# Optimization experiments

Measured on AMD Instinct MI355X. Metric: run time of the kernel, lower is better.

The kernel has to match this reference:

```python
import jax, jax.numpy as jnp
import numpy as np

D_MODEL = 1024
N_HEADS = 16
D_K = D_MODEL // N_HEADS
THETA = 10000.0
NEG_INF = -1e30


def _rope_tables(token_positions, d_k, theta=THETA):
    # freqs[t, i] = t / theta**(2i/d_k), i in [0, d_k/2)
    exponent = jnp.arange(0, d_k, 2, dtype=jnp.float32)  # [d_k/2]
    inv_freq = 1.0 / theta ** (exponent / d_k)
    freqs = token_positions.astype(jnp.float32)[:, None] * inv_freq[None, :]  # [s, d_k/2]
    return jnp.cos(freqs), jnp.sin(freqs)


def _apply_rope(x, cos, sin):
    # x: [..., s, d_k]; interleaved pair rotation (pairs are (x[2i], x[2i+1]))
    x1 = x[..., 0::2]
    x2 = x[..., 1::2]
    r1 = x1 * cos - x2 * sin
    r2 = x1 * sin + x2 * cos
    return jnp.stack([r1, r2], axis=-1).reshape(x.shape)


def setup_inputs() -> dict:
    key = jax.random.key(0)
    ks = jax.random.split(key, 5)
    b, s = 2, 2048
    scale = np.sqrt(2.0 / (D_MODEL + D_MODEL))
    return {
        "x": jax.random.normal(ks[0], (b, s, D_MODEL), dtype=jnp.float32),
        "Wq": jax.random.normal(ks[1], (D_MODEL, D_MODEL), dtype=jnp.float32) * scale,
        "Wk": jax.random.normal(ks[2], (D_MODEL, D_MODEL), dtype=jnp.float32) * scale,
        "Wv": jax.random.normal(ks[3], (D_MODEL, D_MODEL), dtype=jnp.float32) * scale,
        "Wo": jax.random.normal(ks[4], (D_MODEL, D_MODEL), dtype=jnp.float32) * scale,
        "token_positions": jnp.arange(s, dtype=jnp.int64 if jax.config.jax_enable_x64 else jnp.int32),
    }


def reference(x, Wq, Wk, Wv, Wo, token_positions):
    b, s, _ = x.shape
    # QKV projections: weight stored [in, out]
    q = jnp.einsum('bsi,io->bso', x, Wq)
    k = jnp.einsum('bsi,io->bso', x, Wk)
    v = jnp.einsum('bsi,io->bso', x, Wv)
    # split heads: [b, h, s, d_k]
    q = q.reshape(b, s, N_HEADS, D_K).transpose(0, 2, 1, 3)
    k = k.reshape(b, s, N_HEADS, D_K).transpose(0, 2, 1, 3)
    v = v.reshape(b, s, N_HEADS, D_K).transpose(0, 2, 1, 3)
    # RoPE
    cos, sin = _rope_tables(token_positions, D_K)
    q = _apply_rope(q, cos, sin)
    k = _apply_rope(k, cos, sin)
    # causal attention with full materialized scores (faithful to source)
    scores = jnp.einsum('bhid,bhjd->bhij', q, k) / jnp.sqrt(jnp.float32(D_K))
    mask = jnp.tril(jnp.ones((s, s), dtype=bool))
    scores = jnp.where(mask, scores, NEG_INF)
    probs = jax.nn.softmax(scores, axis=-1)
    out = jnp.einsum('bhij,bhjd->bhid', probs, v)
    out = out.transpose(0, 2, 1, 3).reshape(b, s, D_MODEL)
    return jnp.einsum('bsi,io->bso', out, Wo)
```

## Files before the change

kernel.cpp:

```cpp
#include <hip/hip_runtime.h>
#include <hip/hip_bf16.h>
#include <cmath>

#define S_LEN 2048
#define DMODEL 1024
#define NHEADS 16
#define DK 64
#define BATCH 2
#define MTOT (BATCH * S_LEN)

using short8 = __attribute__((ext_vector_type(8))) short;
using floatx4 = __attribute__((ext_vector_type(4))) float;

__device__ __forceinline__ unsigned short f2b(float f) {
    union { float f; unsigned u; } v; v.f = f;
    unsigned r = v.u + 0x7fff + ((v.u >> 16) & 1);
    return (unsigned short)(r >> 16);
}

__device__ __forceinline__ unsigned pack2(float a, float b) {
    float2 t; t.x = a; t.y = b;
    __hip_bfloat162 h = __float22bfloat162_rn(t);
    union { __hip_bfloat162 h; unsigned u; } v; v.h = h;
    return v.u;
}

__device__ __forceinline__ void gload16(const void* g, void* l) {
    __builtin_amdgcn_global_load_lds(
        (const __attribute__((address_space(1))) unsigned int*)g,
        (__attribute__((address_space(3))) unsigned int*)l, 16, 0, 0);
}

#define FENCE() asm volatile("" ::: "memory")

__global__ __launch_bounds__(256) void prep_k(
    const float* __restrict__ x, unsigned short* __restrict__ xb,
    const int* __restrict__ tokpos, float* __restrict__ ct, float* __restrict__ st,
    const float* W0, const float* W1, const float* W2, const float* W3,
    unsigned short* T0, unsigned short* T1, unsigned short* T2, unsigned short* T3) {
    __shared__ float t[64][65];
    const int b = blockIdx.x;
    if (b < 2048) {
        int i = (b * 256 + threadIdx.x) * 8;
        float4 a = *(const float4*)(x + i);
        float4 bb = *(const float4*)(x + i + 4);
        short8 o;
        o[0] = f2b(a.x); o[1] = f2b(a.y); o[2] = f2b(a.z); o[3] = f2b(a.w);
        o[4] = f2b(bb.x); o[5] = f2b(bb.y); o[6] = f2b(bb.z); o[7] = f2b(bb.w);
        *(short8*)(xb + i) = o;
    } else if (b < 2304) {
        int idx = (b - 2048) * 256 + threadIdx.x;
        int si = idx >> 5;
        int ip = idx & 31;
        float pos = (float)tokpos[si];
        float inv_freq = powf(10000.0f, -(float)(2 * ip) / 64.0f);
        float ang = pos * inv_freq;
        ct[idx] = cosf(ang);
        st[idx] = sinf(ang);
    } else {
        int id = b - 2304;
        int z = id >> 8;
        int bx = id & 15, by = (id >> 4) & 15;
        const float* W = z == 0 ? W0 : z == 1 ? W1 : z == 2 ? W2 : W3;
        unsigned short* T = z == 0 ? T0 : z == 1 ? T1 : z == 2 ? T2 : T3;
        const bool perm = (z < 2);
        int n0 = bx * 64, k0 = by * 64;
        int rr = threadIdx.x >> 6, cc = threadIdx.x & 63;
#pragma unroll
        for (int r = 0; r < 16; r++) {
            int row = r * 4 + rr;
            t[row][cc] = W[(size_t)(k0 + row) * DMODEL + n0 + cc];
        }
        __syncthreads();
#pragma unroll
        for (int r = 0; r < 16; r++) {
            int row = r * 4 + rr;
            int drow = perm ? (((row & 1) ? 32 : 0) + (row >> 1)) : row;
            T[(size_t)(n0 + drow) * DMODEL + k0 + cc] = f2b(t[cc][row]);
        }
    }
}

__global__ __launch_bounds__(256) void add_k(float* __restrict__ out,
                                             const float* __restrict__ p) {
    int i = (blockIdx.x * 256 + threadIdx.x) * 8;
    float4 a = *(const float4*)(out + i);
    float4 b = *(const float4*)(p + i);
    float4 c = *(const float4*)(out + i + 4);
    float4 d = *(const float4*)(p + i + 4);
    a.x += b.x; a.y += b.y; a.z += b.z; a.w += b.w;
    c.x += d.x; c.y += d.y; c.z += d.z; c.w += d.w;
    *(float4*)(out + i) = a;
    *(float4*)(out + i + 4) = c;
}

__global__ __launch_bounds__(256) void vtrans_k(const unsigned short* __restrict__ V,
                                                unsigned short* __restrict__ Vt) {
    __shared__ unsigned short t[64][72];
    const int tid = threadIdx.x;
    const int s0 = blockIdx.x * 64, d0 = blockIdx.y * 64;
    const int bb = s0 >> 11;
#pragma unroll
    for (int it = 0; it < 4; it++) {
        int e = (it * 256 + tid) * 4;
        int r = e >> 6, c = e & 63;
        *(ushort4*)&t[r][c] = *(const ushort4*)(V + (size_t)(s0 + r) * DMODEL + d0 + c);
    }
    __syncthreads();
#pragma unroll
    for (int it = 0; it < 4; it++) {
        int e = (it * 256 + tid) * 4;
        int r = e >> 6, c = e & 63;
        ushort4 v;
        v.x = t[c + 0][r]; v.y = t[c + 1][r];
        v.z = t[c + 2][r]; v.w = t[c + 3][r];
        *(ushort4*)(Vt + (size_t)(bb * 1024 + d0 + r) * S_LEN + (s0 & (S_LEN - 1)) + c) = v;
    }
}

__global__ __launch_bounds__(512, 2) void mm_k(
    const unsigned short* __restrict__ A,
    const unsigned short* __restrict__ Bt0, const unsigned short* __restrict__ Bt1,
    const unsigned short* __restrict__ Bt2,
    void* C0, void* C1, void* C2,
    const float* __restrict__ ct, const float* __restrict__ st, int kind) {
    __shared__ __align__(16) unsigned short blob[10 * 8192];

    const int z = blockIdx.z;
    const unsigned short* Bt = (kind == 1) ? Bt0 : (z == 0 ? Bt0 : z == 1 ? Bt1 : Bt2);
    void* C = (kind == 1) ? (z == 0 ? C0 : C1) : (z == 0 ? C0 : z == 1 ? C1 : C2);
    const int mode = (kind == 1) ? 0 : (z == 2 ? 3 : 1);
    const int t0 = (kind == 1) ? z * 8 : 0;
    const int NT = (kind == 1) ? 8 : 16;
    const float qscale = (z == 0 && kind == 0) ? 0.18033688011112042f : 1.0f;

    const int tid = threadIdx.x;
    const int w = tid >> 6, lane = tid & 63;
    const int l15 = lane & 15, quad = lane >> 4;
    const int wr = w >> 2, wc = w & 3;
    const int m0 = blockIdx.x * 256, n0 = blockIdx.y * 256;

    const int rbase = (w >> 1) * 16 + l15;
    const int cbase = (w & 1) * 32 + quad * 8;

    floatx4 acc[8][4];
#pragma unroll
    for (int i = 0; i < 8; i++)
#pragma unroll
        for (int j = 0; j < 4; j++) acc[i][j] = (floatx4){0.f, 0.f, 0.f, 0.f};

    auto stage_half = [&](int h) {
        const int ts = t0 + (h >> 2), part = h & 3;
        const int slot = h % 10;
        const unsigned short* src =
            (part < 2 ? A + (((size_t)(m0 + part * 128 + rbase)) << 10)
                      : Bt + (((size_t)(n0 + (part - 2) * 128 + rbase)) << 10))
            + (size_t)ts * 64 + cbase;
        char* d = (char*)blob + slot * 16384 + w * 1024;
        gload16(src, d);
        gload16(src + (64 << 10), d + 8192);
    };

#pragma unroll
    for (int h = 0; h < 6; ++h) stage_half(h);
    asm volatile("s_waitcnt vmcnt(4)" ::: "memory");
    FENCE(); __builtin_amdgcn_s_barrier(); FENCE();

    short8 af[4][2];
    for (int t = 0; t < NT; ++t) {
        const int sb = (4 * t) % 10;
        int sA = sb + wr;            if (sA >= 10) sA -= 10;
        int sB = sb + 2 + (wc >> 1); if (sB >= 10) sB -= 10;
        const char* LA = (const char*)blob + sA * 16384;
        const char* LB = (const char*)blob + sB * 16384;
#pragma unroll
        for (int q = 0; q < 4; ++q) {
            const int rh = q >> 1, ch = q & 1;
            if (ch == 0) {
#pragma unroll
                for (int ii = 0; ii < 4; ++ii)
#pragma unroll
                    for (int kh = 0; kh < 2; ++kh)
                        af[ii][kh] = *(const short8*)(LA + ((rh * 4 + ii) * 2 + kh) * 1024 + lane * 16);
            }
            short8 bf[2][2];
#pragma unroll
            for (int jj = 0; jj < 2; ++jj)
#pragma unroll
                for (int kh = 0; kh < 2; ++kh)
                    bf[jj][kh] = *(const short8*)(LB + (((wc & 1) * 4 + ch * 2 + jj) * 2 + kh) * 1024 + lane * 16);
            const int h = 4 * t + q + 6;
            if (h < 4 * NT) stage_half(h);
            if (q == 3) {
                if (t == NT - 2) asm volatile("s_waitcnt vmcnt(0)" ::: "memory");
                else             asm volatile("s_waitcnt vmcnt(4)" ::: "memory");
            }
            FENCE(); __builtin_amdgcn_s_barrier(); FENCE();
            __builtin_amdgcn_s_setprio(1);
#pragma unroll
            for (int ii = 0; ii < 4; ++ii)
#pragma unroll
                for (int jj = 0; jj < 2; ++jj) {
                    floatx4 a0 = acc[rh * 4 + ii][ch * 2 + jj];
                    a0 = __builtin_amdgcn_mfma_f32_16x16x32_bf16(af[ii][0], bf[jj][0], a0, 0, 0, 0);
                    a0 = __builtin_amdgcn_mfma_f32_16x16x32_bf16(af[ii][1], bf[jj][1], a0, 0, 0, 0);
                    acc[rh * 4 + ii][ch * 2 + jj] = a0;
                }
            __builtin_amdgcn_s_setprio(0);
            FENCE(); __builtin_amdgcn_s_barrier(); FENCE();
        }
    }

#pragma unroll
    for (int i = 0; i < 8; i++) {
        const int rowb = m0 + wr * 128 + i * 16 + quad * 4;
        if (mode == 0) {
            float* Cf = (float*)C;
#pragma unroll
            for (int j = 0; j < 4; j++) {
                int colb = n0 + wc * 64 + j * 16 + l15;
#pragma unroll
                for (int r = 0; r < 4; r++)
                    Cf[(size_t)(rowb + r) * DMODEL + colb] = acc[i][j][r];
            }
        } else if (mode == 1) {
            unsigned short* Cb = (unsigned short*)C;
#pragma unroll
            for (int jh = 0; jh < 2; jh++) {
                int ip = jh * 16 + l15;
                int cole = n0 + wc * 64 + jh * 16 + l15;
#pragma unroll
                for (int r = 0; r < 4; r++) {
                    int row = rowb + r;
                    int si = row & (S_LEN - 1);
                    float c = ct[si * 32 + ip] * qscale;
                    float s = st[si * 32 + ip] * qscale;
                    float e = acc[i][jh][r];
                    float od = acc[i][jh + 2][r];
                    Cb[(size_t)row * DMODEL + cole] = f2b(e * c - od * s);
                    Cb[(size_t)row * DMODEL + cole + 32] = f2b(e * s + od * c);
                }
            }
        } else {
            unsigned short* Cb = (unsigned short*)C;
#pragma unroll
            for (int j = 0; j < 4; j++) {
                int colb = n0 + wc * 64 + j * 16 + l15;
#pragma unroll
                for (int r = 0; r < 4; r++)
                    Cb[(size_t)(rowb + r) * DMODEL + colb] = f2b(acc[i][j][r]);
            }
        }
    }
}

__global__ __launch_bounds__(256) void attn_k(const unsigned short* __restrict__ Q,
                                              const unsigned short* __restrict__ K,
                                              const unsigned short* __restrict__ Vt,
                                              unsigned short* __restrict__ O) {
    __shared__ __align__(16) unsigned short Kblob[2][4096];
    __shared__ __align__(16) unsigned short Vblob[2][4096];
    __shared__ __align__(16) unsigned short Ps[4][32 * 72];

    const int tid = threadIdx.x;
    const int w = tid >> 6, lane = tid & 63;
    const int l15 = lane & 15, quad = lane >> 4;
    const int idx = blockIdx.x;
    const int qt = 15 - (idx >> 5);
    const int bh = idx & 31;
    const int bb = bh >> 4, h = bh & 15;
    const int qb_w = qt * 128 + w * 32;

    short8 aq[2][2];
#pragma unroll
    for (int qg = 0; qg < 2; qg++) {
        const size_t qoff = (size_t)(bb * S_LEN + qb_w + qg * 16 + l15) * DMODEL + h * DK;
        aq[qg][0] = *(const short8*)(Q + qoff + quad * 8);
        aq[qg][1] = *(const short8*)(Q + qoff + 32 + quad * 8);
    }

    floatx4 o[2][4];
#pragma unroll
    for (int qg = 0; qg < 2; qg++)
#pragma unroll
        for (int f = 0; f < 4; f++) o[qg][f] = (floatx4){0.f, 0.f, 0.f, 0.f};
    float mv[2] = {-1e30f, -1e30f}, lv[2] = {0.f, 0.f};

    const unsigned short* Kb = K + (size_t)(bb * S_LEN) * DMODEL + h * DK;
    const unsigned short* Vb = Vt + (size_t)(bb * 1024 + h * DK) * S_LEN;
    unsigned short* ps = &Ps[w][0];

    auto stage = [&](int b, int kb) {
#pragma unroll
        for (int it = 0; it < 4; it++) {
            int g = it * 4 + w;
            if (g < 8) {
                const unsigned short* gp =
                    Kb + (size_t)(kb + (g >> 1) * 16 + l15) * DMODEL + (g & 1) * 32 + quad * 8;
                gload16(gp, (char*)&Kblob[b][0] + g * 1024);
            } else {
                int gv = g - 8;
                const unsigned short* gp =
                    Vb + (size_t)((gv >> 1) * 16 + l15) * S_LEN + kb + (gv & 1) * 32 + quad * 8;
                gload16(gp, (char*)&Vblob[b][0] + gv * 1024);
            }
        }
    };

    const int nkt = 2 * qt + 2;
    stage(0, 0);
    for (int kt = 0; kt < nkt; kt++) {
        const int b = kt & 1;
        const int kb = kt * 64;
        __syncthreads();
        if (kt + 1 < nkt) stage(b ^ 1, (kt + 1) * 64);

        if (kb <= qb_w + 31) {
            const unsigned short* kbb = &Kblob[b][0];
            floatx4 c[4][2];
            __builtin_amdgcn_s_setprio(1);
#pragma unroll
            for (int g = 0; g < 4; g++) {
                short8 kf0 = *(const short8*)(kbb + (g * 2 + 0) * 512 + lane * 8);
                short8 kf1 = *(const short8*)(kbb + (g * 2 + 1) * 512 + lane * 8);
#pragma unroll
                for (int qg = 0; qg < 2; qg++) {
                    floatx4 t = {0.f, 0.f, 0.f, 0.f};
                    t = __builtin_amdgcn_mfma_f32_16x16x32_bf16(kf0, aq[qg][0], t, 0, 0, 0);
                    c[g][qg] = __builtin_amdgcn_mfma_f32_16x16x32_bf16(kf1, aq[qg][1], t, 0, 0, 0);
                }
            }
            __builtin_amdgcn_s_setprio(0);

#pragma unroll
            for (int qg = 0; qg < 2; qg++) {
                const int qbg = qb_w + qg * 16;
                const int qrow = qbg + l15;
                float sv[16];
                if (kb + 63 <= qbg) {
#pragma unroll
                    for (int g = 0; g < 4; g++)
#pragma unroll
                        for (int r = 0; r < 4; r++) sv[g * 4 + r] = c[g][qg][r];
                } else {
#pragma unroll
                    for (int g = 0; g < 4; g++)
#pragma unroll
                        for (int r = 0; r < 4; r++) {
                            int key = kb + g * 16 + quad * 4 + r;
                            sv[g * 4 + r] = (key <= qrow) ? c[g][qg][r] : -1e30f;
                        }
                }
                float t0 = fmaxf(fmaxf(sv[0], sv[1]), sv[2]);
                float t1 = fmaxf(fmaxf(sv[3], sv[4]), sv[5]);
                float t2 = fmaxf(fmaxf(sv[6], sv[7]), sv[8]);
                float t3 = fmaxf(fmaxf(sv[9], sv[10]), sv[11]);
                float t4 = fmaxf(fmaxf(sv[12], sv[13]), sv[14]);
                float mx = fmaxf(fmaxf(fmaxf(t0, t1), fmaxf(t2, t3)), fmaxf(t4, sv[15]));
                mx = fmaxf(mx, __shfl_xor(mx, 16));
                mx = fmaxf(mx, __shfl_xor(mx, 32));

                if (!__all(mx <= mv[qg])) {
                    float mnew = fmaxf(mv[qg], mx);
                    float alpha = exp2f(mv[qg] - mnew);
                    mv[qg] = mnew;
                    lv[qg] *= alpha;
#pragma unroll
                    for (int f = 0; f < 4; f++) {
                        o[qg][f][0] *= alpha; o[qg][f][1] *= alpha;
                        o[qg][f][2] *= alpha; o[qg][f][3] *= alpha;
                    }
                }
                float p[16], psum = 0.f;
#pragma unroll
                for (int i = 0; i < 16; i++) {
                    p[i] = exp2f(sv[i] - mv[qg]);
                    psum += p[i];
                }
                lv[qg] += psum;

#pragma unroll
                for (int g = 0; g < 4; g++) {
                    uint2 pk;
                    pk.x = pack2(p[g * 4 + 0], p[g * 4 + 1]);
                    pk.y = pack2(p[g * 4 + 2], p[g * 4 + 3]);
                    *(uint2*)(ps + (qg * 16 + l15) * 72 + g * 16 + quad * 4) = pk;
                }
            }

            short8 pf[2][2];
#pragma unroll
            for (int qg = 0; qg < 2; qg++) {
                pf[qg][0] = *(const short8*)(ps + (qg * 16 + l15) * 72 + quad * 8);
                pf[qg][1] = *(const short8*)(ps + (qg * 16 + l15) * 72 + 32 + quad * 8);
            }
            const unsigned short* vbb = &Vblob[b][0];
            __builtin_amdgcn_s_setprio(1);
#pragma unroll
            for (int f = 0; f < 4; f++) {
                short8 vf0 = *(const short8*)(vbb + (f * 2 + 0) * 512 + lane * 8);
                short8 vf1 = *(const short8*)(vbb + (f * 2 + 1) * 512 + lane * 8);
#pragma unroll
                for (int qg = 0; qg < 2; qg++) {
                    o[qg][f] = __builtin_amdgcn_mfma_f32_16x16x32_bf16(vf0, pf[qg][0], o[qg][f], 0, 0, 0);
                    o[qg][f] = __builtin_amdgcn_mfma_f32_16x16x32_bf16(vf1, pf[qg][1], o[qg][f], 0, 0, 0);
                }
            }
            __builtin_amdgcn_s_setprio(0);
        }
    }

#pragma unroll
    for (int qg = 0; qg < 2; qg++) {
        lv[qg] += __shfl_xor(lv[qg], 16);
        lv[qg] += __shfl_xor(lv[qg], 32);
        float inv = 1.0f / lv[qg];
#pragma unroll
        for (int f = 0; f < 4; f++) {
            uint2 pk;
            pk.x = pack2(o[qg][f][0] * inv, o[qg][f][1] * inv);
            pk.y = pack2(o[qg][f][2] * inv, o[qg][f][3] * inv);
            *(uint2*)(ps + (qg * 16 + l15) * 72 + f * 16 + quad * 4) = pk;
        }
        short8 r0 = *(const short8*)(ps + (qg * 16 + l15) * 72 + quad * 8);
        short8 r1 = *(const short8*)(ps + (qg * 16 + l15) * 72 + 32 + quad * 8);
        size_t obase = (size_t)(bb * S_LEN + qb_w + qg * 16 + l15) * DMODEL + h * DK;
        *(short8*)(O + obase + quad * 8) = r0;
        *(short8*)(O + obase + 32 + quad * 8) = r1;
    }
}

extern "C" void kernel_launch(void* const* d_in, const int* in_sizes, int n_in,
                              void* d_out, int out_size, void* d_ws,
                              size_t ws_size, hipStream_t stream) {
    const float* x = (const float*)d_in[0];
    const float* Wq = (const float*)d_in[1];
    const float* Wk = (const float*)d_in[2];
    const float* Wv = (const float*)d_in[3];
    const float* Wo = (const float*)d_in[4];
    const int* tokpos = (const int*)d_in[5];
    float* out = (float*)d_out;

    const size_t MD = (size_t)MTOT * DMODEL;
    const size_t WD = (size_t)DMODEL * DMODEL;
    unsigned short* xb = (unsigned short*)d_ws;
    unsigned short* Wqt = xb + MD;
    unsigned short* Wkt = Wqt + WD;
    unsigned short* Wvt = Wkt + WD;
    unsigned short* Wot = Wvt + WD;
    unsigned short* Q = Wot + WD;
    unsigned short* K = Q + MD;
    unsigned short* V = K + MD;
    unsigned short* Vt = V + MD;
    float* ct = (float*)(Vt + MD);
    float* st = ct + S_LEN * 32;
    unsigned short* O = V;
    float* P1 = (float*)Q;

    prep_k<<<dim3(3328), dim3(256), 0, stream>>>(x, xb, tokpos, ct, st,
                                                 Wq, Wk, Wv, Wo, Wqt, Wkt, Wvt, Wot);

    mm_k<<<dim3(16, 4, 3), dim3(512), 0, stream>>>(xb, Wqt, Wkt, Wvt,
                                                   (void*)Q, (void*)K, (void*)V, ct, st, 0);
    vtrans_k<<<dim3(64, 16), dim3(256), 0, stream>>>(V, Vt);
    attn_k<<<dim3(512), dim3(256), 0, stream>>>(Q, K, Vt, O);
    mm_k<<<dim3(16, 4, 2), dim3(512), 0, stream>>>(O, Wot, Wot, Wot,
                                                   (void*)out, (void*)P1, (void*)P1, ct, st, 1);
    add_k<<<dim3(2048), dim3(256), 0, stream>>>(out, P1);
}
```

Measured before the change: 230.2 us.

## Rebalance causal attention with 256-row tiles, split-KV for long rows, and merge kernel

Attention blocks now cover 256 query rows with 8 waves, and a static table assigns each block a key range. The longest query tiles are split into two key-range halves whose unnormalized partial outputs and max/sum stats go to workspace, and a new merge kernel combines them. The aim is to even out causal work across 352 blocks (11 per batch-head) so the tail of long blocks does not dominate. The cost is an extra kernel launch, fp32 partial-result traffic, and workspace reuse of the xb buffer.

```diff
diff --git a/kernel.cpp b/kernel.cpp
--- a/kernel.cpp
+++ b/kernel.cpp
@@ -254,22 +254,30 @@
     }
 }
 
-__global__ __launch_bounds__(256) void attn_k(const unsigned short* __restrict__ Q,
+__global__ __launch_bounds__(512) void attn_k(const unsigned short* __restrict__ Q,
                                               const unsigned short* __restrict__ K,
                                               const unsigned short* __restrict__ Vt,
-                                              unsigned short* __restrict__ O) {
+                                              unsigned short* __restrict__ O,
+                                              float* __restrict__ Ub,
+                                              float* __restrict__ MLb) {
     __shared__ __align__(16) unsigned short Kblob[2][4096];
     __shared__ __align__(16) unsigned short Vblob[2][4096];
-    __shared__ __align__(16) unsigned short Ps[4][32 * 72];
+    __shared__ __align__(16) unsigned short Ps[8][16 * 72];
+
+    static const int T_j[11]  = {4, 7, 7, 3, 6, 6, 5, 5, 2, 1, 0};
+    static const int T_k0[11] = {0, 0, 16, 0, 0, 14, 0, 12, 0, 0, 0};
+    static const int T_k1[11] = {20, 16, 32, 16, 14, 28, 12, 24, 12, 8, 4};
+    static const int T_sx[11] = {-1, 0, 1, -1, 2, 3, 4, 5, -1, -1, -1};
 
     const int tid = threadIdx.x;
     const int w = tid >> 6, lane = tid & 63;
     const int l15 = lane & 15, quad = lane >> 4;
     const int idx = blockIdx.x;
-    const int qt = 15 - (idx >> 5);
+    const int sr = idx >> 5;
     const int bh = idx & 31;
     const int bb = bh >> 4, h = bh & 15;
-    const int qb_w = qt * 128 + w * 32;
+    const int j = T_j[sr], kt0 = T_k0[sr], kt1 = T_k1[sr], sx = T_sx[sr];
+    const int qb_w = j * 256 + w * 32;
 
     short8 aq[2][2];
 #pragma unroll
@@ -292,8 +300,8 @@
 
     auto stage = [&](int b, int kb) {
 #pragma unroll
-        for (int it = 0; it < 4; it++) {
-            int g = it * 4 + w;
+        for (int it = 0; it < 2; it++) {
+            int g = it * 8 + w;
             if (g < 8) {
                 const unsigned short* gp =
                     Kb + (size_t)(kb + (g >> 1) * 16 + l15) * DMODEL + (g & 1) * 32 + quad * 8;
@@ -307,13 +315,12 @@
         }
     };
 
-    const int nkt = 2 * qt + 2;
-    stage(0, 0);
-    for (int kt = 0; kt < nkt; kt++) {
-        const int b = kt & 1;
+    stage(0, kt0 * 64);
+    for (int kt = kt0; kt < kt1; kt++) {
+        const int b = (kt - kt0) & 1;
         const int kb = kt * 64;
         __syncthreads();
-        if (kt + 1 < nkt) stage(b ^ 1, (kt + 1) * 64);
+        if (kt + 1 < kt1) stage(b ^ 1, (kt + 1) * 64);
 
         if (kb <= qb_w + 31) {
             const unsigned short* kbb = &Kblob[b][0];
@@ -332,6 +339,7 @@
             }
             __builtin_amdgcn_s_setprio(0);
 
+            short8 pf[2][2];
 #pragma unroll
             for (int qg = 0; qg < 2; qg++) {
                 const int qbg = qb_w + qg * 16;
@@ -384,16 +392,12 @@
                     uint2 pk;
                     pk.x = pack2(p[g * 4 + 0], p[g * 4 + 1]);
                     pk.y = pack2(p[g * 4 + 2], p[g * 4 + 3]);
-                    *(uint2*)(ps + (qg * 16 + l15) * 72 + g * 16 + quad * 4) = pk;
-                }
-            }
-
-            short8 pf[2][2];
-#pragma unroll
-            for (int qg = 0; qg < 2; qg++) {
-                pf[qg][0] = *(const short8*)(ps + (qg * 16 + l15) * 72 + quad * 8);
-                pf[qg][1] = *(const short8*)(ps + (qg * 16 + l15) * 72 + 32 + quad * 8);
-            }
+                    *(uint2*)(ps + l15 * 72 + g * 16 + quad * 4) = pk;
+                }
+                pf[qg][0] = *(const short8*)(ps + l15 * 72 + quad * 8);
+                pf[qg][1] = *(const short8*)(ps + l15 * 72 + 32 + quad * 8);
+            }
+
             const unsigned short* vbb = &Vblob[b][0];
             __builtin_amdgcn_s_setprio(1);
 #pragma unroll
@@ -410,24 +414,89 @@
         }
     }
 
-#pragma unroll
-    for (int qg = 0; qg < 2; qg++) {
-        lv[qg] += __shfl_xor(lv[qg], 16);
-        lv[qg] += __shfl_xor(lv[qg], 32);
-        float inv = 1.0f / lv[qg];
-#pragma unroll
-        for (int f = 0; f < 4; f++) {
-            uint2 pk;
-            pk.x = pack2(o[qg][f][0] * inv, o[qg][f][1] * inv);
-            pk.y = pack2(o[qg][f][2] * inv, o[qg][f][3] * inv);
-            *(uint2*)(ps + (qg * 16 + l15) * 72 + f * 16 + quad * 4) = pk;
-        }
-        short8 r0 = *(const short8*)(ps + (qg * 16 + l15) * 72 + quad * 8);
-        short8 r1 = *(const short8*)(ps + (qg * 16 + l15) * 72 + 32 + quad * 8);
-        size_t obase = (size_t)(bb * S_LEN + qb_w + qg * 16 + l15) * DMODEL + h * DK;
-        *(short8*)(O + obase + quad * 8) = r0;
-        *(short8*)(O + obase + 32 + quad * 8) = r1;
-    }
+    if (sx >= 0) {
+        const int slot = sx * 32 + bh;
+#pragma unroll
+        for (int qg = 0; qg < 2; qg++) {
+            float* up = Ub + (size_t)slot * 16384 + (tid * 2 + qg) * 16;
+#pragma unroll
+            for (int f = 0; f < 4; f++) {
+                float4 v; v.x = o[qg][f][0]; v.y = o[qg][f][1];
+                v.z = o[qg][f][2]; v.w = o[qg][f][3];
+                *(float4*)(up + f * 4) = v;
+            }
+            float* mlp = MLb + (size_t)slot * 2048 + (tid * 2 + qg) * 2;
+            mlp[0] = mv[qg];
+            mlp[1] = lv[qg];
+        }
+    } else {
+        __syncthreads();
+#pragma unroll
+        for (int qg = 0; qg < 2; qg++) {
+            float l = lv[qg];
+            l += __shfl_xor(l, 16);
+            l += __shfl_xor(l, 32);
+            float inv = 1.0f / l;
+#pragma unroll
+            for (int f = 0; f < 4; f++) {
+                uint2 pk;
+                pk.x = pack2(o[qg][f][0] * inv, o[qg][f][1] * inv);
+                pk.y = pack2(o[qg][f][2] * inv, o[qg][f][3] * inv);
+                *(uint2*)(ps + l15 * 72 + f * 16 + quad * 4) = pk;
+            }
+            short8 r0 = *(const short8*)(ps + l15 * 72 + quad * 8);
+            short8 r1 = *(const short8*)(ps + l15 * 72 + 32 + quad * 8);
+            size_t obase = (size_t)(bb * S_LEN + qb_w + qg * 16 + l15) * DMODEL + h * DK;
+            *(short8*)(O + obase + quad * 8) = r0;
+            *(short8*)(O + obase + 32 + quad * 8) = r1;
+        }
+    }
+}
+
+__global__ __launch_bounds__(512) void mrg_k(const float* __restrict__ Ub,
+                                             const float* __restrict__ MLb,
+                                             unsigned short* __restrict__ O) {
+    const int pid = blockIdx.x;
+    const int pair = pid >> 5;
+    const int j = 7 - pair;
+    const int bh = pid & 31;
+    const int bb = bh >> 4, h = bh & 15;
+    const int slotA = (pair * 2) * 32 + bh;
+    const int slotB = slotA + 32;
+    const int tid = threadIdx.x;
+    const int q = tid >> 1, dh = tid & 1;
+    const int qg = (q >> 4) & 1;
+    const int tq0 = (q >> 5) * 64 + (q & 15);
+
+    const float* mlA = MLb + (size_t)slotA * 2048;
+    const float* mlB = MLb + (size_t)slotB * 2048;
+    float mA = mlA[(tq0 * 2 + qg) * 2], mB = mlB[(tq0 * 2 + qg) * 2];
+    float lA = 0.f, lB = 0.f;
+#pragma unroll
+    for (int qd = 0; qd < 4; qd++) {
+        int t = ((tq0 + qd * 16) * 2 + qg) * 2 + 1;
+        lA += mlA[t];
+        lB += mlB[t];
+    }
+    float m = fmaxf(mA, mB);
+    float wA = exp2f(mA - m), wB = exp2f(mB - m);
+    float inv = 1.0f / (lA * wA + lB * wB);
+
+    const float* uA = Ub + (size_t)slotA * 16384;
+    const float* uB = Ub + (size_t)slotB * 16384;
+    unsigned short ov[32];
+#pragma unroll
+    for (int dd = 0; dd < 32; dd++) {
+        int d = dh * 32 + dd;
+        int tidq = (q >> 5) * 64 + ((d >> 2) & 3) * 16 + (q & 15);
+        int uoff = (tidq * 2 + qg) * 16 + (d >> 4) * 4 + (d & 3);
+        float v = (uA[uoff] * wA + uB[uoff] * wB) * inv;
+        ov[dd] = f2b(v);
+    }
+    size_t obase = (size_t)(bb * S_LEN + j * 256 + q) * DMODEL + h * DK + dh * 32;
+#pragma unroll
+    for (int c = 0; c < 4; c++)
+        *(short8*)(O + obase + c * 8) = *(short8*)&ov[c * 8];
 }
 
 extern "C" void kernel_launch(void* const* d_in, const int* in_sizes, int n_in,
@@ -456,6 +525,8 @@
     float* st = ct + S_LEN * 32;
     unsigned short* O = V;
     float* P1 = (float*)Q;
+    float* Ub = (float*)xb;
+    float* MLb = Ub + (size_t)192 * 16384;
 
     prep_k<<<dim3(3328), dim3(256), 0, stream>>>(x, xb, tokpos, ct, st,
                                                  Wq, Wk, Wv, Wo, Wqt, Wkt, Wvt, Wot);
@@ -463,7 +534,8 @@
     mm_k<<<dim3(16, 4, 3), dim3(512), 0, stream>>>(xb, Wqt, Wkt, Wvt,
                                                    (void*)Q, (void*)K, (void*)V, ct, st, 0);
     vtrans_k<<<dim3(64, 16), dim3(256), 0, stream>>>(V, Vt);
-    attn_k<<<dim3(512), dim3(256), 0, stream>>>(Q, K, Vt, O);
+    attn_k<<<dim3(352), dim3(512), 0, stream>>>(Q, K, Vt, O, Ub, MLb);
+    mrg_k<<<dim3(96), dim3(512), 0, stream>>>(Ub, MLb, O);
     mm_k<<<dim3(16, 4, 2), dim3(512), 0, stream>>>(O, Wot, Wot, Wot,
                                                    (void*)out, (void*)P1, (void*)P1, ct, st, 1);
     add_k<<<dim3(2048), dim3(256), 0, stream>>>(out, P1);
```

Result: no change. 230.6 us (+0.2%).
